# Kernel tuning notes

Hardware: AMD Instinct MI355X
Metric: run time of the kernel (lower is better)

The kernel has to match this reference:

```python
import jax, jax.numpy as jnp
import numpy as np

N_NODES = 100000
N_EDGES = 1600000
D_IN = 128
D_OUT = 128


def setup_inputs() -> dict:
    key = jax.random.key(0)
    k_x, k_s, k_r, k_w = jax.random.split(key, 4)
    x = jax.random.normal(k_x, (N_NODES, D_IN), dtype=jnp.float32)
    senders = jax.random.randint(k_s, (N_EDGES,), 0, N_NODES, dtype=jnp.int32)
    receivers = jax.random.randint(k_r, (N_EDGES,), 0, N_NODES, dtype=jnp.int32)
    # xavier_uniform for (D_IN, D_OUT)
    limit = float(np.sqrt(6.0 / (D_IN + D_OUT)))
    weight = jax.random.uniform(k_w, (D_IN, D_OUT), dtype=jnp.float32,
                                minval=-limit, maxval=limit)
    bias = jnp.zeros((D_OUT,), dtype=jnp.float32)
    return {"x": x, "senders": senders, "receivers": receivers,
            "n_node": N_NODES, "weight": weight, "bias": bias}


def reference(x, senders, receivers, n_node, weight, bias):
    # Linear node update: [N, D_in] @ [D_in, D_out] + bias
    h = jnp.dot(x, weight) + bias
    total_num_nodes = x.shape[0]

    # Degree counts via segment_sum of ones (symmetric normalization)
    ones = jnp.ones_like(senders)
    sender_degree = jax.ops.segment_sum(ones, senders, num_segments=total_num_nodes)
    receiver_degree = jax.ops.segment_sum(ones, receivers, num_segments=total_num_nodes)

    # Pre-scale by 1/sqrt(deg_out), scatter-sum along edges, post-scale by 1/sqrt(deg_in)
    h = h * jax.lax.rsqrt(jnp.maximum(sender_degree, 1.0))[:, None]
    agg = jax.ops.segment_sum(h[senders], receivers, num_segments=total_num_nodes)
    out = agg * jax.lax.rsqrt(jnp.maximum(receiver_degree, 1.0))[:, None]
    return out
```

## Files before the change

kernel.cpp:

```cpp
#include <hip/hip_runtime.h>
#include <hip/hip_bf16.h>
#include <stdint.h>

#define N_NODES 100000
#define N_EDGES 1600000
#define NB 196
#define BCAP 9216
#define TILE2 4096
#define BIN2_BLOCKS ((N_EDGES + TILE2 - 1) / TILE2)

static const size_t OFF_H      = 0;
static const size_t OFF_SSCALE = 25600000;
static const size_t OFF_ROWP   = 26000000;
static const size_t OFF_ROWE   = 26400000;
static const size_t OFF_SDEG   = 26800000;
static const size_t OFF_RCUR   = 27200000;
static const size_t OFF_WFRAG  = 27201024;
static const size_t OFF_EBUF   = 27233792;

using short8 = __attribute__((ext_vector_type(8))) short;
using f32x4  = __attribute__((ext_vector_type(4))) float;

static __device__ __forceinline__ short f2bf(float f) {
    uint32_t u = __float_as_uint(f);
    uint32_t r = (u + 0x7fffu + ((u >> 16) & 1u)) >> 16;
    return (short)r;
}

__global__ __launch_bounds__(256) void init_kernel(int* __restrict__ rcur) {
    rcur[threadIdx.x] = threadIdx.x * BCAP;
}

__global__ __launch_bounds__(256) void prep_w_kernel(const float* __restrict__ W,
                                                     short8* __restrict__ wfrag) {
    int slot = blockIdx.x * 256 + threadIdx.x;
    int f = slot >> 6, lane = slot & 63;
    int quad = lane >> 4, mcol = lane & 15;
    int s = f >> 3, c = f & 7;
    int krow = s * 32 + quad * 8;
    int ncol = c * 16 + mcol;
    short8 wf;
    #pragma unroll
    for (int j = 0; j < 8; j++)
        wf[j] = f2bf(W[(krow + j) * 128 + ncol]);
    wfrag[slot] = wf;
}

__global__ __launch_bounds__(256) void binr_kernel(const int* __restrict__ snd,
                                                   const int* __restrict__ rcv,
                                                   int* __restrict__ rcur,
                                                   int* __restrict__ sdeg,
                                                   uint32_t* __restrict__ ebuf) {
    __shared__ int hist[256];
    __shared__ int coff[256];
    __shared__ int ccur[256];
    __shared__ int gbase[256];
    __shared__ uint32_t stage[TILE2];

    const int t = threadIdx.x;
    const int base = blockIdx.x * TILE2;

    uint32_t ss[16], rs[16];
    #pragma unroll
    for (int j = 0; j < 16; j++) {
        int idx = base + j * 256 + t;
        bool ok = idx < N_EDGES;
        ss[j] = ok ? (uint32_t)snd[idx] : 0u;
        rs[j] = ok ? (uint32_t)rcv[idx] : 0xffffffffu;
    }

    #pragma unroll
    for (int j = 0; j < 16; j++)
        if (rs[j] != 0xffffffffu) atomicAdd(&sdeg[ss[j]], 1);

    hist[t] = 0;
    __syncthreads();
    #pragma unroll
    for (int j = 0; j < 16; j++)
        if (rs[j] != 0xffffffffu) atomicAdd(&hist[rs[j] >> 9], 1);
    __syncthreads();

    int v = hist[t];
    ccur[t] = v;
    __syncthreads();
    #pragma unroll
    for (int off = 1; off < 256; off <<= 1) {
        int tv = (t >= off) ? ccur[t - off] : 0;
        __syncthreads();
        ccur[t] += tv;
        __syncthreads();
    }
    int excl = ccur[t] - v;
    coff[t] = excl;
    int gb = 0;
    if (v > 0) gb = atomicAdd(&rcur[t], v);
    gbase[t] = gb - excl;
    __syncthreads();
    ccur[t] = excl;
    __syncthreads();

    #pragma unroll
    for (int j = 0; j < 16; j++) {
        uint32_t r = rs[j];
        if (r != 0xffffffffu) {
            int pos = atomicAdd(&ccur[r >> 9], 1);
            stage[pos] = (ss[j] << 9) | (r & 511u);
        }
    }
    __syncthreads();

    int total = coff[255] + hist[255];
    for (int i = t; i < total; i += 256) {
        uint32_t pv = stage[i];
        int lo = 0;
        #pragma unroll
        for (int step = 128; step; step >>= 1)
            if (lo + step < 256 && coff[lo + step] <= i) lo += step;
        ebuf[gbase[lo] + i] = pv;
    }
}

__global__ __launch_bounds__(256) void bucket_kernel(const int* __restrict__ rcur,
                                                     uint32_t* __restrict__ ebuf,
                                                     const int* __restrict__ sdeg,
                                                     int* __restrict__ row_ptr,
                                                     int* __restrict__ row_end,
                                                     float* __restrict__ sscale) {
    __shared__ int hist_l[512];
    __shared__ int excl_l[512];
    __shared__ int cur_l[512];
    __shared__ int ps[256];
    __shared__ uint32_t inb[BCAP];
    __shared__ uint32_t perm[BCAP];

    const int b = blockIdx.x;
    const int t = threadIdx.x;
    const int nbase = b << 9;
    const int base = b * BCAP;
    const int size = rcur[b] - base;

    hist_l[t] = 0; hist_l[t + 256] = 0;
    __syncthreads();

    for (int i = t; i < size; i += 256) {
        uint32_t v = ebuf[base + i];
        inb[i] = v;
        atomicAdd(&hist_l[v & 511u], 1);
    }
    __syncthreads();

    int h0 = hist_l[2 * t], h1 = hist_l[2 * t + 1];
    int p = h0 + h1;
    ps[t] = p;
    __syncthreads();
    #pragma unroll
    for (int off = 1; off < 256; off <<= 1) {
        int tv = (t >= off) ? ps[t - off] : 0;
        __syncthreads();
        ps[t] += tv;
        __syncthreads();
    }
    int pe = ps[t] - p;
    excl_l[2 * t] = pe;
    excl_l[2 * t + 1] = pe + h0;
    cur_l[2 * t] = pe;
    cur_l[2 * t + 1] = pe + h0;
    __syncthreads();

    for (int i = t; i < 512; i += 256) {
        int n = nbase + i;
        if (n < N_NODES) {
            int s = base + excl_l[i];
            row_ptr[n] = s;
            row_end[n] = s + hist_l[i];
            sscale[n] = rsqrtf(fmaxf((float)sdeg[n], 1.f));
        }
    }

    for (int i = t; i < size; i += 256) {
        uint32_t v = inb[i];
        int pos = atomicAdd(&cur_l[v & 511u], 1);
        perm[pos] = v >> 9;
    }
    __syncthreads();
    for (int i = t; i < size; i += 256)
        ebuf[base + i] = perm[i];
}

__global__ __launch_bounds__(256, 3) void gemm_mfma_kernel(const float* __restrict__ x,
                                                           const short8* __restrict__ wfrag,
                                                           const float* __restrict__ bias,
                                                           const float* __restrict__ sscale,
                                                           short* __restrict__ h) {
    const int t = threadIdx.x;
    const int lane = t & 63;
    const int wv = t >> 6;
    const int quad = lane >> 4;
    const int mcol = lane & 15;

    const int node0 = blockIdx.x * 128 + wv * 32;
    short8 afrag[2][4];
    #pragma unroll
    for (int mf = 0; mf < 2; mf++) {
        int node = node0 + mf * 16 + mcol;
        bool ok = node < N_NODES;
        const float* xr = x + (size_t)(ok ? node : 0) * 128;
        #pragma unroll
        for (int s = 0; s < 4; s++) {
            int k0 = s * 32 + quad * 8;
            f32x4 v0 = ok ? *(const f32x4*)(xr + k0)     : f32x4{0.f,0.f,0.f,0.f};
            f32x4 v1 = ok ? *(const f32x4*)(xr + k0 + 4) : f32x4{0.f,0.f,0.f,0.f};
            short8 af;
            #pragma unroll
            for (int j = 0; j < 4; j++) {
                af[j]     = f2bf(v0[j]);
                af[4 + j] = f2bf(v1[j]);
            }
            afrag[mf][s] = af;
        }
    }

    f32x4 acc[2][8];
    #pragma unroll
    for (int mf = 0; mf < 2; mf++)
        #pragma unroll
        for (int c = 0; c < 8; c++)
            acc[mf][c] = f32x4{0.f, 0.f, 0.f, 0.f};

    #pragma unroll
    for (int s = 0; s < 4; s++) {
        #pragma unroll
        for (int c = 0; c < 8; c++) {
            short8 bfrag = wfrag[(s * 8 + c) * 64 + lane];
            acc[0][c] = __builtin_amdgcn_mfma_f32_16x16x32_bf16(afrag[0][s], bfrag, acc[0][c], 0, 0, 0);
            acc[1][c] = __builtin_amdgcn_mfma_f32_16x16x32_bf16(afrag[1][s], bfrag, acc[1][c], 0, 0, 0);
        }
    }

    float rsv[2][4];
    #pragma unroll
    for (int mf = 0; mf < 2; mf++)
        #pragma unroll
        for (int r = 0; r < 4; r++) {
            int nd = node0 + mf * 16 + quad * 4 + r;
            rsv[mf][r] = (nd < N_NODES) ? sscale[nd] : 1.f;
        }

    #pragma unroll
    for (int mf = 0; mf < 2; mf++)
        #pragma unroll
        for (int c = 0; c < 8; c++) {
            float bval = bias[c * 16 + mcol];
            #pragma unroll
            for (int r = 0; r < 4; r++) {
                int nd = node0 + mf * 16 + quad * 4 + r;
                if (nd < N_NODES)
                    h[(size_t)nd * 128 + c * 16 + mcol] =
                        f2bf((acc[mf][c][r] + bval) * rsv[mf][r]);
            }
        }
}

__global__ __launch_bounds__(256) void gather_kernel(const uint32_t* __restrict__ h2,
                                                     const int* __restrict__ row_ptr,
                                                     const int* __restrict__ row_end,
                                                     const uint32_t* __restrict__ esrc,
                                                     f32x4* __restrict__ out4) {
    const int wv = threadIdx.x >> 6;
    const int lane = threadIdx.x & 63;
    const int sub = lane >> 4;
    const int ln = lane & 15;
    const int node = blockIdx.x * 16 + wv * 4 + sub;

    const int b = row_ptr[node];
    const int e = row_end[node];

    float a0 = 0.f, a1 = 0.f, a2 = 0.f, a3 = 0.f;
    float a4 = 0.f, a5 = 0.f, a6 = 0.f, a7 = 0.f;

    int i = b;
    for (; i + 4 <= e; i += 4) {
        uint32_t s0 = esrc[i + 0], s1 = esrc[i + 1], s2 = esrc[i + 2], s3 = esrc[i + 3];
        uint4 v0 = *(const uint4*)&h2[(size_t)s0 * 64 + ln * 4];
        uint4 v1 = *(const uint4*)&h2[(size_t)s1 * 64 + ln * 4];
        uint4 v2 = *(const uint4*)&h2[(size_t)s2 * 64 + ln * 4];
        uint4 v3 = *(const uint4*)&h2[(size_t)s3 * 64 + ln * 4];
        a0 += __uint_as_float(v0.x << 16) + __uint_as_float(v1.x << 16)
            + __uint_as_float(v2.x << 16) + __uint_as_float(v3.x << 16);
        a1 += __uint_as_float(v0.x & 0xffff0000u) + __uint_as_float(v1.x & 0xffff0000u)
            + __uint_as_float(v2.x & 0xffff0000u) + __uint_as_float(v3.x & 0xffff0000u);
        a2 += __uint_as_float(v0.y << 16) + __uint_as_float(v1.y << 16)
            + __uint_as_float(v2.y << 16) + __uint_as_float(v3.y << 16);
        a3 += __uint_as_float(v0.y & 0xffff0000u) + __uint_as_float(v1.y & 0xffff0000u)
            + __uint_as_float(v2.y & 0xffff0000u) + __uint_as_float(v3.y & 0xffff0000u);
        a4 += __uint_as_float(v0.z << 16) + __uint_as_float(v1.z << 16)
            + __uint_as_float(v2.z << 16) + __uint_as_float(v3.z << 16);
        a5 += __uint_as_float(v0.z & 0xffff0000u) + __uint_as_float(v1.z & 0xffff0000u)
            + __uint_as_float(v2.z & 0xffff0000u) + __uint_as_float(v3.z & 0xffff0000u);
        a6 += __uint_as_float(v0.w << 16) + __uint_as_float(v1.w << 16)
            + __uint_as_float(v2.w << 16) + __uint_as_float(v3.w << 16);
        a7 += __uint_as_float(v0.w & 0xffff0000u) + __uint_as_float(v1.w & 0xffff0000u)
            + __uint_as_float(v2.w & 0xffff0000u) + __uint_as_float(v3.w & 0xffff0000u);
    }
    for (; i < e; i++) {
        uint32_t s = esrc[i];
        uint4 v = *(const uint4*)&h2[(size_t)s * 64 + ln * 4];
        a0 += __uint_as_float(v.x << 16);
        a1 += __uint_as_float(v.x & 0xffff0000u);
        a2 += __uint_as_float(v.y << 16);
        a3 += __uint_as_float(v.y & 0xffff0000u);
        a4 += __uint_as_float(v.z << 16);
        a5 += __uint_as_float(v.z & 0xffff0000u);
        a6 += __uint_as_float(v.w << 16);
        a7 += __uint_as_float(v.w & 0xffff0000u);
    }
    float rs = rsqrtf(fmaxf((float)(e - b), 1.f));
    f32x4 o0 = {a0 * rs, a1 * rs, a2 * rs, a3 * rs};
    f32x4 o1 = {a4 * rs, a5 * rs, a6 * rs, a7 * rs};
    out4[(size_t)node * 32 + ln * 2 + 0] = o0;
    out4[(size_t)node * 32 + ln * 2 + 1] = o1;
}

extern "C" void kernel_launch(void* const* d_in, const int* in_sizes, int n_in,
                              void* d_out, int out_size, void* d_ws, size_t ws_size,
                              hipStream_t stream) {
    const float* x    = (const float*)d_in[0];
    const int*   snd  = (const int*)d_in[1];
    const int*   rcv  = (const int*)d_in[2];
    const float* W    = (const float*)d_in[4];
    const float* bias = (const float*)d_in[5];

    char* ws = (char*)d_ws;
    short*    h      = (short*)(ws + OFF_H);
    float*    sscale = (float*)(ws + OFF_SSCALE);
    int*      rowp   = (int*)(ws + OFF_ROWP);
    int*      rowe   = (int*)(ws + OFF_ROWE);
    int*      sdeg   = (int*)(ws + OFF_SDEG);
    int*      rcur   = (int*)(ws + OFF_RCUR);
    short8*   wfrag  = (short8*)(ws + OFF_WFRAG);
    uint32_t* ebuf   = (uint32_t*)(ws + OFF_EBUF);

    hipMemsetAsync(ws + OFF_SDEG, 0, 400000, stream);

    init_kernel    <<<1, 256, 0, stream>>>(rcur);
    prep_w_kernel  <<<8, 256, 0, stream>>>(W, wfrag);
    binr_kernel    <<<BIN2_BLOCKS, 256, 0, stream>>>(snd, rcv, rcur, sdeg, ebuf);
    bucket_kernel  <<<NB, 256, 0, stream>>>(rcur, ebuf, sdeg, rowp, rowe, sscale);
    gemm_mfma_kernel<<<(N_NODES + 127) / 128, 256, 0, stream>>>(x, wfrag, bias, sscale, h);
    gather_kernel  <<<N_NODES / 16, 256, 0, stream>>>((const uint32_t*)h, rowp, rowe, ebuf, (f32x4*)d_out);
}
```

Before: 283.0 us.

## Restructure edge bucketing into coarse 49-bucket pass and 782-block fine sort

Replaces the 196-bucket binning and per-bucket counting sort with two passes. A coarse pass bins edges into 49 buckets of 2048 receivers. Then 782 fine blocks each filter their 128-receiver slice out of a coarse bucket and counting-sort it into CSR. This gives more, smaller fine blocks, which should raise parallelism and cut shared-memory use, and the coarse scatter becomes wave-per-bucket contiguous copies. The cost is that each coarse bucket is scanned 16 times by the fine blocks, and fixed FCAP capacity could overflow on skewed inputs. ebuf1 also aliases the h buffer region.

```diff
diff --git a/kernel.cpp b/kernel.cpp
--- a/kernel.cpp
+++ b/kernel.cpp
@@ -4,19 +4,22 @@
 
 #define N_NODES 100000
 #define N_EDGES 1600000
-#define NB 196
-#define BCAP 9216
-#define TILE2 4096
-#define BIN2_BLOCKS ((N_EDGES + TILE2 - 1) / TILE2)
+#define CB 49
+#define CCAP 34816
+#define T1 4096
+#define P1_BLOCKS ((N_EDGES + T1 - 1) / T1)
+#define FB 782
+#define FCAP 2560
 
 static const size_t OFF_H      = 0;
+static const size_t OFF_EBUF1  = 0;
 static const size_t OFF_SSCALE = 25600000;
 static const size_t OFF_ROWP   = 26000000;
 static const size_t OFF_ROWE   = 26400000;
 static const size_t OFF_SDEG   = 26800000;
-static const size_t OFF_RCUR   = 27200000;
+static const size_t OFF_CCUR   = 27200000;
 static const size_t OFF_WFRAG  = 27201024;
-static const size_t OFF_EBUF   = 27233792;
+static const size_t OFF_EBUF2  = 27233792;
 
 using short8 = __attribute__((ext_vector_type(8))) short;
 using f32x4  = __attribute__((ext_vector_type(4))) float;
@@ -27,8 +30,8 @@
     return (short)r;
 }
 
-__global__ __launch_bounds__(256) void init_kernel(int* __restrict__ rcur) {
-    rcur[threadIdx.x] = threadIdx.x * BCAP;
+__global__ __launch_bounds__(64) void init_kernel(int* __restrict__ ccur) {
+    if (threadIdx.x < CB) ccur[threadIdx.x] = threadIdx.x * CCAP;
 }
 
 __global__ __launch_bounds__(256) void prep_w_kernel(const float* __restrict__ W,
@@ -46,19 +49,20 @@
     wfrag[slot] = wf;
 }
 
-__global__ __launch_bounds__(256) void binr_kernel(const int* __restrict__ snd,
-                                                   const int* __restrict__ rcv,
-                                                   int* __restrict__ rcur,
-                                                   int* __restrict__ sdeg,
-                                                   uint32_t* __restrict__ ebuf) {
-    __shared__ int hist[256];
-    __shared__ int coff[256];
-    __shared__ int ccur[256];
-    __shared__ int gbase[256];
-    __shared__ uint32_t stage[TILE2];
+__global__ __launch_bounds__(256) void coarse_kernel(const int* __restrict__ snd,
+                                                     const int* __restrict__ rcv,
+                                                     int* __restrict__ ccur,
+                                                     int* __restrict__ sdeg,
+                                                     uint32_t* __restrict__ ebuf1) {
+    __shared__ int hist[64];
+    __shared__ int sc[64];
+    __shared__ int coff[64];
+    __shared__ int gb[64];
+    __shared__ int cur[64];
+    __shared__ uint32_t stage[T1];
 
     const int t = threadIdx.x;
-    const int base = blockIdx.x * TILE2;
+    const int base = blockIdx.x * T1;
 
     uint32_t ss[16], rs[16];
     #pragma unroll
@@ -73,118 +77,118 @@
     for (int j = 0; j < 16; j++)
         if (rs[j] != 0xffffffffu) atomicAdd(&sdeg[ss[j]], 1);
 
-    hist[t] = 0;
+    if (t < 64) hist[t] = 0;
     __syncthreads();
     #pragma unroll
     for (int j = 0; j < 16; j++)
-        if (rs[j] != 0xffffffffu) atomicAdd(&hist[rs[j] >> 9], 1);
-    __syncthreads();
-
-    int v = hist[t];
-    ccur[t] = v;
-    __syncthreads();
-    #pragma unroll
-    for (int off = 1; off < 256; off <<= 1) {
-        int tv = (t >= off) ? ccur[t - off] : 0;
+        if (rs[j] != 0xffffffffu) atomicAdd(&hist[rs[j] >> 11], 1);
+    __syncthreads();
+
+    if (t < 64) sc[t] = hist[t];
+    __syncthreads();
+    #pragma unroll
+    for (int off = 1; off < 64; off <<= 1) {
+        int v_ = 0;
+        if (t < 64 && t >= off) v_ = sc[t - off];
         __syncthreads();
-        ccur[t] += tv;
+        if (t < 64) sc[t] += v_;
         __syncthreads();
     }
-    int excl = ccur[t] - v;
-    coff[t] = excl;
-    int gb = 0;
-    if (v > 0) gb = atomicAdd(&rcur[t], v);
-    gbase[t] = gb - excl;
-    __syncthreads();
-    ccur[t] = excl;
+    if (t < 64) {
+        int excl = sc[t] - hist[t];
+        coff[t] = excl;
+        cur[t] = excl;
+        gb[t] = (hist[t] > 0) ? atomicAdd(&ccur[t], hist[t]) : 0;
+    }
     __syncthreads();
 
     #pragma unroll
     for (int j = 0; j < 16; j++) {
         uint32_t r = rs[j];
         if (r != 0xffffffffu) {
-            int pos = atomicAdd(&ccur[r >> 9], 1);
-            stage[pos] = (ss[j] << 9) | (r & 511u);
-        }
-    }
-    __syncthreads();
-
-    int total = coff[255] + hist[255];
-    for (int i = t; i < total; i += 256) {
-        uint32_t pv = stage[i];
-        int lo = 0;
-        #pragma unroll
-        for (int step = 128; step; step >>= 1)
-            if (lo + step < 256 && coff[lo + step] <= i) lo += step;
-        ebuf[gbase[lo] + i] = pv;
-    }
-}
-
-__global__ __launch_bounds__(256) void bucket_kernel(const int* __restrict__ rcur,
-                                                     uint32_t* __restrict__ ebuf,
-                                                     const int* __restrict__ sdeg,
-                                                     int* __restrict__ row_ptr,
-                                                     int* __restrict__ row_end,
-                                                     float* __restrict__ sscale) {
-    __shared__ int hist_l[512];
-    __shared__ int excl_l[512];
-    __shared__ int cur_l[512];
-    __shared__ int ps[256];
-    __shared__ uint32_t inb[BCAP];
-    __shared__ uint32_t perm[BCAP];
-
-    const int b = blockIdx.x;
+            int b = r >> 11;
+            int pos = atomicAdd(&cur[b], 1);
+            stage[pos] = (ss[j] << 11) | (r & 2047u);
+        }
+    }
+    __syncthreads();
+
+    const int wv = t >> 6, ln = t & 63;
+    for (int b = wv; b < CB; b += 4) {
+        int cnt = hist[b], off = coff[b], g = gb[b];
+        for (int i = ln; i < cnt; i += 64)
+            ebuf1[g + i] = stage[off + i];
+    }
+}
+
+__global__ __launch_bounds__(256) void fine_kernel(const int* __restrict__ ccur,
+                                                   const uint32_t* __restrict__ ebuf1,
+                                                   const int* __restrict__ sdeg,
+                                                   uint32_t* __restrict__ ebuf2,
+                                                   int* __restrict__ row_ptr,
+                                                   int* __restrict__ row_end,
+                                                   float* __restrict__ sscale) {
+    __shared__ int hist[128];
+    __shared__ int sc[128];
+    __shared__ int cur[128];
+    __shared__ int lcnt;
+    __shared__ uint32_t inb[FCAP];
+    __shared__ uint32_t perm[FCAP];
+
+    const int f = blockIdx.x;
     const int t = threadIdx.x;
-    const int nbase = b << 9;
-    const int base = b * BCAP;
-    const int size = rcur[b] - base;
-
-    hist_l[t] = 0; hist_l[t + 256] = 0;
-    __syncthreads();
-
-    for (int i = t; i < size; i += 256) {
-        uint32_t v = ebuf[base + i];
-        inb[i] = v;
-        atomicAdd(&hist_l[v & 511u], 1);
-    }
-    __syncthreads();
-
-    int h0 = hist_l[2 * t], h1 = hist_l[2 * t + 1];
-    int p = h0 + h1;
-    ps[t] = p;
-    __syncthreads();
-    #pragma unroll
-    for (int off = 1; off < 256; off <<= 1) {
-        int tv = (t >= off) ? ps[t - off] : 0;
+    const int c = f >> 4;
+    const uint32_t sub = (uint32_t)(f & 15);
+    const int cbase = c * CCAP;
+    const int csize = ccur[c] - cbase;
+
+    if (t < 128) hist[t] = 0;
+    if (t == 0) lcnt = 0;
+    __syncthreads();
+
+    for (int i = t; i < csize; i += 256) {
+        uint32_t v = ebuf1[cbase + i];
+        if (((v >> 7) & 15u) == sub) {
+            int p = atomicAdd(&lcnt, 1);
+            inb[p] = v;
+            atomicAdd(&hist[v & 127u], 1);
+        }
+    }
+    __syncthreads();
+
+    const int cnt = lcnt;
+
+    if (t < 128) sc[t] = hist[t];
+    __syncthreads();
+    #pragma unroll
+    for (int off = 1; off < 128; off <<= 1) {
+        int v_ = 0;
+        if (t < 128 && t >= off) v_ = sc[t - off];
         __syncthreads();
-        ps[t] += tv;
+        if (t < 128) sc[t] += v_;
         __syncthreads();
     }
-    int pe = ps[t] - p;
-    excl_l[2 * t] = pe;
-    excl_l[2 * t + 1] = pe + h0;
-    cur_l[2 * t] = pe;
-    cur_l[2 * t + 1] = pe + h0;
-    __syncthreads();
-
-    for (int i = t; i < 512; i += 256) {
-        int n = nbase + i;
+    if (t < 128) {
+        int excl = sc[t] - hist[t];
+        cur[t] = excl;
+        int n = f * 128 + t;
         if (n < N_NODES) {
-            int s = base + excl_l[i];
+            int s = f * FCAP + excl;
             row_ptr[n] = s;
-            row_end[n] = s + hist_l[i];
+            row_end[n] = s + hist[t];
             sscale[n] = rsqrtf(fmaxf((float)sdeg[n], 1.f));
         }
     }
-
-    for (int i = t; i < size; i += 256) {
+    __syncthreads();
+
+    for (int i = t; i < cnt; i += 256) {
         uint32_t v = inb[i];
-        int pos = atomicAdd(&cur_l[v & 511u], 1);
-        perm[pos] = v >> 9;
-    }
-    __syncthreads();
-    for (int i = t; i < size; i += 256)
-        ebuf[base + i] = perm[i];
+        int pos = atomicAdd(&cur[v & 127u], 1);
+        perm[pos] = v >> 11;
+    }
+    __syncthreads();
+    for (int i = t; i < cnt; i += 256)
+        ebuf2[f * FCAP + i] = perm[i];
 }
 
 __global__ __launch_bounds__(256, 3) void gemm_mfma_kernel(const float* __restrict__ x,
@@ -332,20 +336,21 @@
 
     char* ws = (char*)d_ws;
     short*    h      = (short*)(ws + OFF_H);
+    uint32_t* ebuf1  = (uint32_t*)(ws + OFF_EBUF1);
     float*    sscale = (float*)(ws + OFF_SSCALE);
     int*      rowp   = (int*)(ws + OFF_ROWP);
     int*      rowe   = (int*)(ws + OFF_ROWE);
     int*      sdeg   = (int*)(ws + OFF_SDEG);
-    int*      rcur   = (int*)(ws + OFF_RCUR);
+    int*      ccur   = (int*)(ws + OFF_CCUR);
     short8*   wfrag  = (short8*)(ws + OFF_WFRAG);
-    uint32_t* ebuf   = (uint32_t*)(ws + OFF_EBUF);
+    uint32_t* ebuf2  = (uint32_t*)(ws + OFF_EBUF2);
 
     hipMemsetAsync(ws + OFF_SDEG, 0, 400000, stream);
 
-    init_kernel    <<<1, 256, 0, stream>>>(rcur);
+    init_kernel    <<<1, 64, 0, stream>>>(ccur);
     prep_w_kernel  <<<8, 256, 0, stream>>>(W, wfrag);
-    binr_kernel    <<<BIN2_BLOCKS, 256, 0, stream>>>(snd, rcv, rcur, sdeg, ebuf);
-    bucket_kernel  <<<NB, 256, 0, stream>>>(rcur, ebuf, sdeg, rowp, rowe, sscale);
+    coarse_kernel  <<<P1_BLOCKS, 256, 0, stream>>>(snd, rcv, ccur, sdeg, ebuf1);
+    fine_kernel    <<<FB, 256, 0, stream>>>(ccur, ebuf1, sdeg, ebuf2, rowp, rowe, sscale);
     gemm_mfma_kernel<<<(N_NODES + 127) / 128, 256, 0, stream>>>(x, wfrag, bias, sscale, h);
-    gather_kernel  <<<N_NODES / 16, 256, 0, stream>>>((const uint32_t*)h, rowp, rowe, ebuf, (f32x4*)d_out);
-}
+    gather_kernel  <<<N_NODES / 16, 256, 0, stream>>>((const uint32_t*)h, rowp, rowe, ebuf2, (f32x4*)d_out);
+}
```

Result: slower. 321.8 us (+13.7%).
